# Kernel optimization log

Hardware: AMD Instinct MI355X
Metric: run time of the kernel (lower is better)

Reference implementation:

```python
import jax, jax.numpy as jnp
import numpy as np

N, E = 50000, 250000          # nodes, edges
IN, OUT, EDIM = 9, 84, 1      # NNConv(9, 84), edge nn Linear(1, 9*84)
EPS = 1e-5                    # BatchNorm1d default eps


def setup_inputs() -> dict:
    key = jax.random.key(0)
    ks = jax.random.split(key, 8)
    return {
        "x": jax.random.normal(ks[0], (N, IN), jnp.float32),
        "edge_index": jax.random.randint(ks[1], (2, E), 0, N, dtype=jnp.int64),
        "edge_attr": jax.random.normal(ks[2], (E, EDIM), jnp.float32),
        # edge nn: Linear(EDIM, IN*OUT) generating per-edge weight matrices
        "nn_w": jax.random.normal(ks[3], (EDIM, IN * OUT), jnp.float32) * (1.0 / np.sqrt(EDIM)),
        "nn_b": jnp.zeros((IN * OUT,), jnp.float32),
        # NNConv root weight + bias
        "root": jax.random.normal(ks[4], (IN, OUT), jnp.float32) * (1.0 / np.sqrt(IN)),
        "bias": jnp.zeros((OUT,), jnp.float32),
        # BatchNorm1d(84) affine params
        "gamma": jnp.ones((OUT,), jnp.float32),
        "beta": jnp.zeros((OUT,), jnp.float32),
    }


def reference(x, edge_index, edge_attr, nn_w, nn_b, root, bias, gamma, beta):
    src, dst = edge_index[0], edge_index[1]
    # per-edge weight matrices: [E, IN, OUT]
    w_e = (edge_attr @ nn_w + nn_b).reshape(E, IN, OUT)
    # gather source node features and apply edge-specific matmul: [E, OUT]
    msg = jnp.einsum('ei,eio->eo', x[src], w_e)
    # scatter-add to destination nodes (NNConv default aggr='add'): [N, OUT]
    aggr = jax.ops.segment_sum(msg, dst, num_segments=N)
    out = x @ root + aggr + bias
    # BatchNorm1d(84), training mode (biased batch stats)
    mean = out.mean(0)
    var = out.var(0)
    out = (out - mean) * jax.lax.rsqrt(var + EPS) * gamma + beta
    return out
```

## Files before the change

kernel.cpp:

```cpp
#include <hip/hip_runtime.h>

#define N_NODES 50000
#define E_EDGES 250000
#define IN_F 9
#define OUT_F 84
#define GROUPS 21
#define BN_EPS 1e-5f

#define STATS_OFF 0
#define HEAD_OFF  256
#define NEXT_OFF  50256
#define S_OFF     300256

#define STATS_BLOCKS 336
#define STATS_THREADS 256
#define STATS_TOTAL (STATS_BLOCKS * STATS_THREADS)

__global__ void init_ws_kernel(float* __restrict__ stats, int* __restrict__ head) {
    int i = blockIdx.x * blockDim.x + threadIdx.x;
    if (i < 2 * OUT_F) stats[i] = 0.0f;
    if (i < N_NODES) head[i] = -1;
}

__global__ void build_list_kernel(const int* __restrict__ ei,
                                  int* __restrict__ head,
                                  int* __restrict__ next) {
    int e = blockIdx.x * blockDim.x + threadIdx.x;
    if (e >= E_EDGES) return;
    int dst = ei[E_EDGES + e];
    next[e] = atomicExch(&head[dst], e);
}

__global__ void gather_kernel(const float* __restrict__ x,
                              const int* __restrict__ ei,
                              const float* __restrict__ ea,
                              const int* __restrict__ head,
                              const int* __restrict__ next,
                              float* __restrict__ S) {
    int gid = blockIdx.x * blockDim.x + threadIdx.x;
    if (gid >= N_NODES * IN_F) return;
    int n = gid / IN_F;
    int i = gid - n * IN_F;

    float s0 = 0.0f, s1 = 0.0f;
    int e = head[n];
    while (e >= 0) {
        int src = ei[e];
        float a = ea[e];
        float xv = x[src * IN_F + i];
        s0 += xv;
        s1 += a * xv;
        e = next[e];
    }
    S[n * 18 + i] = s0;
    S[n * 18 + 9 + i] = s1;
}

__global__ void node_kernel(const float* __restrict__ x,
                            const float* __restrict__ S,
                            const float* __restrict__ nw,
                            const float* __restrict__ nb,
                            const float* __restrict__ root,
                            const float* __restrict__ bias,
                            float* __restrict__ out) {
    __shared__ __align__(16) float4 Ws[IN_F * GROUPS];
    __shared__ __align__(16) float4 Bs[IN_F * GROUPS];
    __shared__ __align__(16) float4 Rs[IN_F * GROUPS];
    __shared__ __align__(16) float4 bs[GROUPS];
    for (int t = threadIdx.x; t < IN_F * GROUPS; t += blockDim.x) {
        Ws[t] = ((const float4*)nw)[t];
        Bs[t] = ((const float4*)nb)[t];
        Rs[t] = ((const float4*)root)[t];
    }
    if (threadIdx.x < GROUPS) bs[threadIdx.x] = ((const float4*)bias)[threadIdx.x];
    __syncthreads();

    int gid = blockIdx.x * blockDim.x + threadIdx.x;
    if (gid >= N_NODES * GROUPS) return;
    int n = gid / GROUPS;
    int g = gid - n * GROUPS;

    float xv[IN_F], s0[IN_F], s1[IN_F];
#pragma unroll
    for (int i = 0; i < IN_F; ++i) {
        xv[i] = x[n * IN_F + i];
        s0[i] = S[n * 18 + i];
        s1[i] = S[n * 18 + 9 + i];
    }

    float4 acc = bs[g];
#pragma unroll
    for (int i = 0; i < IN_F; ++i) {
        float4 r = Rs[i * GROUPS + g];
        float4 w = Ws[i * GROUPS + g];
        float4 b = Bs[i * GROUPS + g];
        acc.x += xv[i] * r.x + s1[i] * w.x + s0[i] * b.x;
        acc.y += xv[i] * r.y + s1[i] * w.y + s0[i] * b.y;
        acc.z += xv[i] * r.z + s1[i] * w.z + s0[i] * b.z;
        acc.w += xv[i] * r.w + s1[i] * w.w + s0[i] * b.w;
    }
    *(float4*)&out[gid * 4] = acc;
}

__global__ void stats_kernel(const float* __restrict__ out,
                             float* __restrict__ stats) {
    __shared__ float sbin[2 * OUT_F];
    if (threadIdx.x < 2 * OUT_F) sbin[threadIdx.x] = 0.0f;
    __syncthreads();

    const int gid0 = blockIdx.x * blockDim.x + threadIdx.x;
    const int g = gid0 % GROUPS;

    float4 s = make_float4(0.f, 0.f, 0.f, 0.f);
    float4 q = make_float4(0.f, 0.f, 0.f, 0.f);
    for (int f = gid0; f < N_NODES * GROUPS; f += STATS_TOTAL) {
        float4 v = ((const float4*)out)[f];
        s.x += v.x; s.y += v.y; s.z += v.z; s.w += v.w;
        q.x += v.x * v.x; q.y += v.y * v.y;
        q.z += v.z * v.z; q.w += v.w * v.w;
    }

    atomicAdd(&sbin[g * 4 + 0], s.x);
    atomicAdd(&sbin[g * 4 + 1], s.y);
    atomicAdd(&sbin[g * 4 + 2], s.z);
    atomicAdd(&sbin[g * 4 + 3], s.w);
    atomicAdd(&sbin[OUT_F + g * 4 + 0], q.x);
    atomicAdd(&sbin[OUT_F + g * 4 + 1], q.y);
    atomicAdd(&sbin[OUT_F + g * 4 + 2], q.z);
    atomicAdd(&sbin[OUT_F + g * 4 + 3], q.w);
    __syncthreads();

    if (threadIdx.x < 2 * OUT_F)
        atomicAdd(&stats[threadIdx.x], sbin[threadIdx.x]);
}

__global__ void norm_kernel(float* __restrict__ out,
                            const float* __restrict__ stats,
                            const float* __restrict__ gamma,
                            const float* __restrict__ beta) {
    int gid = blockIdx.x * blockDim.x + threadIdx.x;
    if (gid >= N_NODES * GROUPS) return;
    int g = gid % GROUPS;

    const float inv_n = 1.0f / (float)N_NODES;
    float4 s = *(const float4*)&stats[g * 4];
    float4 q = *(const float4*)&stats[OUT_F + g * 4];
    float4 gm = *(const float4*)&gamma[g * 4];
    float4 bt = *(const float4*)&beta[g * 4];

    float4 v = *(float4*)&out[gid * 4];

    float mx = s.x * inv_n, my = s.y * inv_n, mz = s.z * inv_n, mw = s.w * inv_n;
    float ix = rsqrtf(q.x * inv_n - mx * mx + BN_EPS) * gm.x;
    float iy = rsqrtf(q.y * inv_n - my * my + BN_EPS) * gm.y;
    float iz = rsqrtf(q.z * inv_n - mz * mz + BN_EPS) * gm.z;
    float iw = rsqrtf(q.w * inv_n - mw * mw + BN_EPS) * gm.w;

    v.x = (v.x - mx) * ix + bt.x;
    v.y = (v.y - my) * iy + bt.y;
    v.z = (v.z - mz) * iz + bt.z;
    v.w = (v.w - mw) * iw + bt.w;

    *(float4*)&out[gid * 4] = v;
}

extern "C" void kernel_launch(void* const* d_in, const int* in_sizes, int n_in,
                              void* d_out, int out_size, void* d_ws, size_t ws_size,
                              hipStream_t stream) {
    const float* x     = (const float*)d_in[0];
    const int*   ei    = (const int*)d_in[1];
    const float* ea    = (const float*)d_in[2];
    const float* nw    = (const float*)d_in[3];
    const float* nb    = (const float*)d_in[4];
    const float* root  = (const float*)d_in[5];
    const float* bias  = (const float*)d_in[6];
    const float* gamma = (const float*)d_in[7];
    const float* beta  = (const float*)d_in[8];
    float*       out   = (float*)d_out;

    float* wsf   = (float*)d_ws;
    int*   wsi   = (int*)d_ws;
    float* stats = wsf + STATS_OFF;
    int*   head  = wsi + HEAD_OFF;
    int*   next  = wsi + NEXT_OFF;
    float* S     = wsf + S_OFF;

    init_ws_kernel<<<(N_NODES + 255) / 256, 256, 0, stream>>>(stats, head);
    build_list_kernel<<<(E_EDGES + 255) / 256, 256, 0, stream>>>(ei, head, next);
    gather_kernel<<<(N_NODES * IN_F + 255) / 256, 256, 0, stream>>>(x, ei, ea, head, next, S);
    node_kernel<<<(N_NODES * GROUPS + 255) / 256, 256, 0, stream>>>(x, S, nw, nb, root, bias, out);
    stats_kernel<<<STATS_BLOCKS, STATS_THREADS, 0, stream>>>(out, stats);
    norm_kernel<<<(N_NODES * GROUPS + 255) / 256, 256, 0, stream>>>(out, stats, gamma, beta);
}
```

Measured before the change: 132.1 us.

## Fuse gather, node transform and BN stats into one tiled kernel

Merges the linked-list gather, per-node linear transform and batch-statistics reduction into one kernel that handles 24 nodes per block. The gathered sums stay in shared memory and the column sums are accumulated from registers, so the intermediate S buffer and the extra full read of out by a separate stats pass go away. The workspace init kernel becomes a memset plus a stats zero-out folded into build_list. In exchange only 216 of 256 threads do the serial edge-list walk, and more blocks each do a global atomic flush of the stats.

```diff
diff --git a/kernel.cpp b/kernel.cpp
--- a/kernel.cpp
+++ b/kernel.cpp
@@ -7,131 +7,113 @@
 #define GROUPS 21
 #define BN_EPS 1e-5f
 
+#define NB_TILE 24
+#define NTILES ((N_NODES + NB_TILE - 1) / NB_TILE)
+
 #define STATS_OFF 0
 #define HEAD_OFF  256
 #define NEXT_OFF  50256
-#define S_OFF     300256
-
-#define STATS_BLOCKS 336
-#define STATS_THREADS 256
-#define STATS_TOTAL (STATS_BLOCKS * STATS_THREADS)
-
-__global__ void init_ws_kernel(float* __restrict__ stats, int* __restrict__ head) {
-    int i = blockIdx.x * blockDim.x + threadIdx.x;
-    if (i < 2 * OUT_F) stats[i] = 0.0f;
-    if (i < N_NODES) head[i] = -1;
-}
 
 __global__ void build_list_kernel(const int* __restrict__ ei,
                                   int* __restrict__ head,
-                                  int* __restrict__ next) {
+                                  int* __restrict__ next,
+                                  float* __restrict__ stats) {
     int e = blockIdx.x * blockDim.x + threadIdx.x;
-    if (e >= E_EDGES) return;
-    int dst = ei[E_EDGES + e];
-    next[e] = atomicExch(&head[dst], e);
+    if (blockIdx.x == 0 && threadIdx.x < 2 * OUT_F) stats[threadIdx.x] = 0.0f;
+    if (e < E_EDGES) {
+        int dst = ei[E_EDGES + e];
+        next[e] = atomicExch(&head[dst], e);
+    }
 }
 
-__global__ void gather_kernel(const float* __restrict__ x,
-                              const int* __restrict__ ei,
-                              const float* __restrict__ ea,
-                              const int* __restrict__ head,
-                              const int* __restrict__ next,
-                              float* __restrict__ S) {
-    int gid = blockIdx.x * blockDim.x + threadIdx.x;
-    if (gid >= N_NODES * IN_F) return;
-    int n = gid / IN_F;
-    int i = gid - n * IN_F;
-
-    float s0 = 0.0f, s1 = 0.0f;
-    int e = head[n];
-    while (e >= 0) {
-        int src = ei[e];
-        float a = ea[e];
-        float xv = x[src * IN_F + i];
-        s0 += xv;
-        s1 += a * xv;
-        e = next[e];
-    }
-    S[n * 18 + i] = s0;
-    S[n * 18 + 9 + i] = s1;
-}
-
-__global__ void node_kernel(const float* __restrict__ x,
-                            const float* __restrict__ S,
-                            const float* __restrict__ nw,
-                            const float* __restrict__ nb,
-                            const float* __restrict__ root,
-                            const float* __restrict__ bias,
-                            float* __restrict__ out) {
+__global__ void fused_kernel(const float* __restrict__ x,
+                             const int*   __restrict__ ei,
+                             const float* __restrict__ ea,
+                             const float* __restrict__ nw,
+                             const float* __restrict__ nb,
+                             const float* __restrict__ root,
+                             const float* __restrict__ bias,
+                             const int*   __restrict__ head,
+                             const int*   __restrict__ next,
+                             float* __restrict__ out,
+                             float* __restrict__ stats) {
     __shared__ __align__(16) float4 Ws[IN_F * GROUPS];
     __shared__ __align__(16) float4 Bs[IN_F * GROUPS];
     __shared__ __align__(16) float4 Rs[IN_F * GROUPS];
-    __shared__ __align__(16) float4 bs[GROUPS];
-    for (int t = threadIdx.x; t < IN_F * GROUPS; t += blockDim.x) {
+    __shared__ __align__(16) float4 bs4[GROUPS];
+    __shared__ float Stile[NB_TILE * 18];
+    __shared__ float Xtile[NB_TILE * IN_F];
+    __shared__ float sbin[2 * OUT_F];
+
+    const int tid = threadIdx.x;
+    for (int t = tid; t < IN_F * GROUPS; t += blockDim.x) {
         Ws[t] = ((const float4*)nw)[t];
         Bs[t] = ((const float4*)nb)[t];
         Rs[t] = ((const float4*)root)[t];
     }
-    if (threadIdx.x < GROUPS) bs[threadIdx.x] = ((const float4*)bias)[threadIdx.x];
+    if (tid < GROUPS) bs4[tid] = ((const float4*)bias)[tid];
+    if (tid < 2 * OUT_F) sbin[tid] = 0.0f;
+
+    const int nbase = blockIdx.x * NB_TILE;
+
+    if (tid < NB_TILE * IN_F) {
+        int nl = tid / IN_F, i = tid - nl * IN_F;
+        int n = nbase + nl;
+        float s0 = 0.f, s1 = 0.f;
+        if (n < N_NODES) {
+            Xtile[nl * IN_F + i] = x[n * IN_F + i];
+            for (int e = head[n]; (unsigned)e < E_EDGES; e = next[e]) {
+                float xv = x[ei[e] * IN_F + i];
+                s0 += xv;
+                s1 += ea[e] * xv;
+            }
+        }
+        Stile[nl * 18 + i]     = s0;
+        Stile[nl * 18 + 9 + i] = s1;
+    }
     __syncthreads();
 
-    int gid = blockIdx.x * blockDim.x + threadIdx.x;
-    if (gid >= N_NODES * GROUPS) return;
-    int n = gid / GROUPS;
-    int g = gid - n * GROUPS;
-
-    float xv[IN_F], s0[IN_F], s1[IN_F];
+    float4 sa = make_float4(0.f, 0.f, 0.f, 0.f);
+    float4 qa = make_float4(0.f, 0.f, 0.f, 0.f);
+    const int g = tid % GROUPS;
+    if (tid < 252) {
 #pragma unroll
-    for (int i = 0; i < IN_F; ++i) {
-        xv[i] = x[n * IN_F + i];
-        s0[i] = S[n * 18 + i];
-        s1[i] = S[n * 18 + 9 + i];
+        for (int k = 0; k < 2; ++k) {
+            int p  = tid + k * 252;
+            int nl = p / GROUPS;
+            int n  = nbase + nl;
+            if (n < N_NODES) {
+                float4 acc = bs4[g];
+#pragma unroll
+                for (int i = 0; i < IN_F; ++i) {
+                    float xv = Xtile[nl * IN_F + i];
+                    float s0 = Stile[nl * 18 + i];
+                    float s1 = Stile[nl * 18 + 9 + i];
+                    float4 r = Rs[i * GROUPS + g];
+                    float4 w = Ws[i * GROUPS + g];
+                    float4 b = Bs[i * GROUPS + g];
+                    acc.x += xv * r.x + s1 * w.x + s0 * b.x;
+                    acc.y += xv * r.y + s1 * w.y + s0 * b.y;
+                    acc.z += xv * r.z + s1 * w.z + s0 * b.z;
+                    acc.w += xv * r.w + s1 * w.w + s0 * b.w;
+                }
+                *(float4*)&out[n * OUT_F + g * 4] = acc;
+                sa.x += acc.x; sa.y += acc.y; sa.z += acc.z; sa.w += acc.w;
+                qa.x += acc.x * acc.x; qa.y += acc.y * acc.y;
+                qa.z += acc.z * acc.z; qa.w += acc.w * acc.w;
+            }
+        }
+        atomicAdd(&sbin[g * 4 + 0], sa.x);
+        atomicAdd(&sbin[g * 4 + 1], sa.y);
+        atomicAdd(&sbin[g * 4 + 2], sa.z);
+        atomicAdd(&sbin[g * 4 + 3], sa.w);
+        atomicAdd(&sbin[OUT_F + g * 4 + 0], qa.x);
+        atomicAdd(&sbin[OUT_F + g * 4 + 1], qa.y);
+        atomicAdd(&sbin[OUT_F + g * 4 + 2], qa.z);
+        atomicAdd(&sbin[OUT_F + g * 4 + 3], qa.w);
     }
-
-    float4 acc = bs[g];
-#pragma unroll
-    for (int i = 0; i < IN_F; ++i) {
-        float4 r = Rs[i * GROUPS + g];
-        float4 w = Ws[i * GROUPS + g];
-        float4 b = Bs[i * GROUPS + g];
-        acc.x += xv[i] * r.x + s1[i] * w.x + s0[i] * b.x;
-        acc.y += xv[i] * r.y + s1[i] * w.y + s0[i] * b.y;
-        acc.z += xv[i] * r.z + s1[i] * w.z + s0[i] * b.z;
-        acc.w += xv[i] * r.w + s1[i] * w.w + s0[i] * b.w;
-    }
-    *(float4*)&out[gid * 4] = acc;
-}
-
-__global__ void stats_kernel(const float* __restrict__ out,
-                             float* __restrict__ stats) {
-    __shared__ float sbin[2 * OUT_F];
-    if (threadIdx.x < 2 * OUT_F) sbin[threadIdx.x] = 0.0f;
     __syncthreads();
-
-    const int gid0 = blockIdx.x * blockDim.x + threadIdx.x;
-    const int g = gid0 % GROUPS;
-
-    float4 s = make_float4(0.f, 0.f, 0.f, 0.f);
-    float4 q = make_float4(0.f, 0.f, 0.f, 0.f);
-    for (int f = gid0; f < N_NODES * GROUPS; f += STATS_TOTAL) {
-        float4 v = ((const float4*)out)[f];
-        s.x += v.x; s.y += v.y; s.z += v.z; s.w += v.w;
-        q.x += v.x * v.x; q.y += v.y * v.y;
-        q.z += v.z * v.z; q.w += v.w * v.w;
-    }
-
-    atomicAdd(&sbin[g * 4 + 0], s.x);
-    atomicAdd(&sbin[g * 4 + 1], s.y);
-    atomicAdd(&sbin[g * 4 + 2], s.z);
-    atomicAdd(&sbin[g * 4 + 3], s.w);
-    atomicAdd(&sbin[OUT_F + g * 4 + 0], q.x);
-    atomicAdd(&sbin[OUT_F + g * 4 + 1], q.y);
-    atomicAdd(&sbin[OUT_F + g * 4 + 2], q.z);
-    atomicAdd(&sbin[OUT_F + g * 4 + 3], q.w);
-    __syncthreads();
-
-    if (threadIdx.x < 2 * OUT_F)
-        atomicAdd(&stats[threadIdx.x], sbin[threadIdx.x]);
+    if (tid < 2 * OUT_F) atomicAdd(&stats[tid], sbin[tid]);
 }
 
 __global__ void norm_kernel(float* __restrict__ out,
@@ -183,12 +165,10 @@
     float* stats = wsf + STATS_OFF;
     int*   head  = wsi + HEAD_OFF;
     int*   next  = wsi + NEXT_OFF;
-    float* S     = wsf + S_OFF;
 
-    init_ws_kernel<<<(N_NODES + 255) / 256, 256, 0, stream>>>(stats, head);
-    build_list_kernel<<<(E_EDGES + 255) / 256, 256, 0, stream>>>(ei, head, next);
-    gather_kernel<<<(N_NODES * IN_F + 255) / 256, 256, 0, stream>>>(x, ei, ea, head, next, S);
-    node_kernel<<<(N_NODES * GROUPS + 255) / 256, 256, 0, stream>>>(x, S, nw, nb, root, bias, out);
-    stats_kernel<<<STATS_BLOCKS, STATS_THREADS, 0, stream>>>(out, stats);
+    hipMemsetAsync(head, 0xFF, N_NODES * sizeof(int), stream);
+    build_list_kernel<<<(E_EDGES + 255) / 256, 256, 0, stream>>>(ei, head, next, stats);
+    fused_kernel<<<NTILES, 256, 0, stream>>>(x, ei, ea, nw, nb, root, bias,
+                                             head, next, out, stats);
     norm_kernel<<<(N_NODES * GROUPS + 255) / 256, 256, 0, stream>>>(out, stats, gamma, beta);
 }
```

New measurement: 166.1 us. +25.7%, slower.
